# Kernel tuning notes

Hardware: AMD Instinct MI355X
Metric: run time of the kernel (lower is better)

Reference implementation:

```python
import jax, jax.numpy as jnp
import numpy as np

NUM_MODELS = 4
B = 16384
HIDDEN = 512
QDIM = 256
LAST_HIDDEN = 256
UW = 0.1          # uncertainty_weight
EPS = 1e-5        # LayerNorm eps (torch default)
FEAT_DIMS = [1024, 768, 512, 640]


def _linear(x, W, b):
    return x @ W.T + b


def _layernorm(h, g, b):
    mu = jnp.mean(h, axis=-1, keepdims=True)
    var = jnp.mean((h - mu) ** 2, axis=-1, keepdims=True)
    return (h - mu) * jax.lax.rsqrt(var + EPS) * g + b


def setup_inputs() -> dict:
    key = jax.random.key(0)
    ks = jax.random.split(key, 40)
    inp = {}
    for i, d in enumerate(FEAT_DIMS):
        inp[f"feat{i}"] = jax.random.normal(ks[i], (B, d), jnp.float32)
        inp[f"W_intra{i}"] = jax.random.normal(ks[4 + i], (HIDDEN, d), jnp.float32) / np.sqrt(d)
        inp[f"b_intra{i}"] = jnp.zeros((HIDDEN,), jnp.float32)
    inp["pred_scores"] = jax.random.uniform(ks[8], (B, NUM_MODELS), jnp.float32)
    inp["pred_vars"] = jax.random.uniform(ks[9], (B, NUM_MODELS), jnp.float32)
    inp["ln_g"] = jnp.ones((HIDDEN,), jnp.float32)
    inp["ln_b"] = jnp.zeros((HIDDEN,), jnp.float32)
    inp["Wq"] = jax.random.normal(ks[10], (QDIM, HIDDEN), jnp.float32) / np.sqrt(HIDDEN)
    inp["bq"] = jnp.zeros((QDIM,), jnp.float32)
    inp["Wk"] = jax.random.normal(ks[11], (QDIM, HIDDEN), jnp.float32) / np.sqrt(HIDDEN)
    inp["bk"] = jnp.zeros((QDIM,), jnp.float32)
    inp["Wv"] = jax.random.normal(ks[12], (QDIM, HIDDEN), jnp.float32) / np.sqrt(HIDDEN)
    inp["bv"] = jnp.zeros((QDIM,), jnp.float32)
    d1 = NUM_MODELS * QDIM + NUM_MODELS
    inp["W1"] = jax.random.normal(ks[13], (LAST_HIDDEN, d1), jnp.float32) / np.sqrt(d1)
    inp["b1"] = jnp.zeros((LAST_HIDDEN,), jnp.float32)
    inp["Wfc"] = jax.random.normal(ks[14], (1, LAST_HIDDEN), jnp.float32) / np.sqrt(LAST_HIDDEN)
    inp["bfc"] = jnp.zeros((1,), jnp.float32)
    return inp


def _forward(feats, pred_scores, pred_vars, W_intras, b_intras,
             ln_g, ln_b, Wq, bq, Wk, bk, Wv, bv, W1, b1, Wfc, bfc):
    # per-model branch: Linear -> ReLU -> (dropout=id) -> ReLU -> LayerNorm
    hiddens = []
    for i in range(NUM_MODELS):
        h = jax.nn.relu(_linear(feats[i], W_intras[i], b_intras[i]))
        h = jax.nn.relu(h)  # second relu after dropout (identity in eval)
        hiddens.append(_layernorm(h, ln_g, ln_b))
    H = jnp.stack(hiddens, axis=1)  # (B, M, HIDDEN)

    # cross-attention with uncertainty; NOTE source bug: key = drop(q) => keys == queries
    q = jnp.einsum('bmh,qh->bmq', H, Wq) + bq          # (B, M, Q)
    k = q                                              # faithful to `key = self.drop(q)`
    v = jnp.einsum('bmh,qh->bmq', H, Wv) + bv          # (B, M, Q)

    scores = jnp.einsum('biq,bjq->bij', q, k)          # (B, M, M)
    vars_ = pred_vars[:, None, :] + pred_vars[:, :, None]  # vars[b,i,j] = v[b,j] + v[b,i]
    scores = jax.nn.softmax(scores - UW * vars_, axis=-1)
    z = jnp.einsum('bij,bjq->biq', scores, v).reshape(B, NUM_MODELS * QDIM)

    out = jnp.concatenate([z, pred_scores], axis=-1)
    out = _linear(out, W1, b1)
    logits = _linear(out, Wfc, bfc)
    return jax.nn.sigmoid(logits)  # (B, 1)


def reference(feat0, feat1, feat2, feat3,
              W_intra0, b_intra0, W_intra1, b_intra1,
              W_intra2, b_intra2, W_intra3, b_intra3,
              pred_scores, pred_vars, ln_g, ln_b,
              Wq, bq, Wk, bk, Wv, bv, W1, b1, Wfc, bfc):
    feats = [feat0, feat1, feat2, feat3]
    W_intras = [W_intra0, W_intra1, W_intra2, W_intra3]
    b_intras = [b_intra0, b_intra1, b_intra2, b_intra3]
    return _forward(feats, pred_scores, pred_vars, W_intras, b_intras,
                    ln_g, ln_b, Wq, bq, Wk, bk, Wv, bv, W1, b1, Wfc, bfc)
```

## Files before the change

kernel.cpp:

```cpp
#include <hip/hip_runtime.h>
#include <hip/hip_bf16.h>


typedef __bf16 bf16;
typedef __bf16 bf16x4_t __attribute__((ext_vector_type(4)));
typedef __bf16 bf16x8_t __attribute__((ext_vector_type(8)));
typedef float  f32x4_t  __attribute__((ext_vector_type(4)));

__device__ __forceinline__ bf16x8_t cvt8(f32x4_t a, f32x4_t b) {
  bf16x8_t r;
  r[0] = (bf16)a[0]; r[1] = (bf16)a[1]; r[2] = (bf16)a[2]; r[3] = (bf16)a[3];
  r[4] = (bf16)b[0]; r[5] = (bf16)b[1]; r[6] = (bf16)b[2]; r[7] = (bf16)b[3];
  return r;
}

__device__ __forceinline__ void gl_lds16(const void* g, void* l) {
  __builtin_amdgcn_global_load_lds(
      (const __attribute__((address_space(1))) void*)g,
      (__attribute__((address_space(3))) void*)l, 16, 0, 0);
}

#define SBAR()   __builtin_amdgcn_s_barrier()
#define SCHED0() __builtin_amdgcn_sched_barrier(0)

__device__ __forceinline__ bf16x8_t frag_b16(const bf16* Ts, int row, int c0) {
  const int byte = row * 64 + ((c0 ^ ((row >> 1) & 3)) << 4);
  return *(const bf16x8_t*)((const char*)Ts + byte);
}
__device__ __forceinline__ bf16x8_t frag_f32(const float* Ts, int row, int g) {
  const int p0 = (2 * g)     ^ (row & 7);
  const int p1 = (2 * g + 1) ^ (row & 7);
  f32x4_t lo = *(const f32x4_t*)((const char*)Ts + row * 128 + (p0 << 4));
  f32x4_t hi = *(const f32x4_t*)((const char*)Ts + row * 128 + (p1 << 4));
  return cvt8(lo, hi);
}

__device__ __forceinline__ void stage_b16(const bf16* __restrict__ src, int ld,
                                          int k0, bf16* lds) {
  const int l = threadIdx.x & 63;
  const int w = threadIdx.x >> 6;
#pragma unroll
  for (int j = 0; j < 2; ++j) {
    const int rb = w * 32 + j * 16;
    const int r  = rb + (l >> 2);
    const int sc = (l & 3) ^ ((r >> 1) & 3);
    gl_lds16(src + (size_t)r * ld + k0 + sc * 8, (char*)lds + rb * 64);
  }
}
__device__ __forceinline__ void stage_f32(const float* __restrict__ src, int ld,
                                          int k0, float* lds) {
  const int l = threadIdx.x & 63;
  const int w = threadIdx.x >> 6;
#pragma unroll
  for (int j = 0; j < 4; ++j) {
    const int rb = w * 32 + j * 8;
    const int r  = rb + (l >> 3);
    const int q  = (l & 7) ^ (r & 7);
    gl_lds16(src + (size_t)r * ld + k0 + q * 4, (char*)lds + rb * 128);
  }
}

template<int AF32>
__device__ __forceinline__ void stage_deep(const void* A, int lda, const void* B,
                                           int ldb, int k0, char* buf) {
  if (AF32) {
    stage_f32((const float*)A, lda, k0, (float*)buf);
    stage_b16((const bf16*)B, ldb, k0, (bf16*)(buf + 16384));
  } else {
    stage_b16((const bf16*)A, lda, k0, (bf16*)buf);
    stage_f32((const float*)B, ldb, k0, (float*)(buf + 8192));
  }
}

template<int AF32>
__device__ __forceinline__ void mfma_deep(const char* buf, f32x4_t acc[4][4]) {
  const int lane = threadIdx.x & 63;
  const int wid  = threadIdx.x >> 6;
  const int wm = wid >> 1, wn = wid & 1;
  const int fr = lane & 15, g = lane >> 4;
  bf16x8_t ar[4], br[4];
  if (AF32) {
    const float* Af = (const float*)buf;
    const bf16*  Bb = (const bf16*)(buf + 16384);
#pragma unroll
    for (int mi = 0; mi < 4; ++mi) ar[mi] = frag_f32(Af, wm * 64 + mi * 16 + fr, g);
#pragma unroll
    for (int ni = 0; ni < 4; ++ni) br[ni] = frag_b16(Bb, wn * 64 + ni * 16 + fr, g);
  } else {
    const bf16*  Ab = (const bf16*)buf;
    const float* Bf = (const float*)(buf + 8192);
#pragma unroll
    for (int mi = 0; mi < 4; ++mi) ar[mi] = frag_b16(Ab, wm * 64 + mi * 16 + fr, g);
#pragma unroll
    for (int ni = 0; ni < 4; ++ni) br[ni] = frag_f32(Bf, wn * 64 + ni * 16 + fr, g);
  }
#pragma unroll
  for (int mi = 0; mi < 4; ++mi)
#pragma unroll
    for (int ni = 0; ni < 4; ++ni)
      acc[mi][ni] = __builtin_amdgcn_mfma_f32_16x16x32_bf16(ar[mi], br[ni], acc[mi][ni], 0, 0, 0);
}

template<int AF32>
__device__ __forceinline__ void core_deep3(const void* A, int lda, const void* B,
                                           int ldb, int K, char* lds,
                                           f32x4_t acc[4][4]) {
  const int nt = K >> 5;
  stage_deep<AF32>(A, lda, B, ldb, 0,  lds);
  stage_deep<AF32>(A, lda, B, ldb, 32, lds + 24576);
  stage_deep<AF32>(A, lda, B, ldb, 64, lds + 49152);
  int buf = 0;
  for (int t = 0; t < nt; ++t) {
    const int ahead = nt - 1 - t;
    if (ahead >= 2)      asm volatile("s_waitcnt vmcnt(12)" ::: "memory");
    else if (ahead == 1) asm volatile("s_waitcnt vmcnt(6)"  ::: "memory");
    else                 asm volatile("s_waitcnt vmcnt(0)"  ::: "memory");
    SBAR(); SCHED0();
    __builtin_amdgcn_s_setprio(1);
    mfma_deep<AF32>(lds + buf * 24576, acc);
    __builtin_amdgcn_s_setprio(0);
    SCHED0(); SBAR();
    if (t + 3 < nt) stage_deep<AF32>(A, lda, B, ldb, (t + 3) * 32, lds + buf * 24576);
    buf = (buf == 2) ? 0 : buf + 1;
  }
}

template<int RELU>
__device__ __forceinline__ void epi_bf16(f32x4_t acc[4][4], bf16* __restrict__ C, int ldc,
                                         const float* __restrict__ bias) {
  const int lane = threadIdx.x & 63;
  const int wid  = threadIdx.x >> 6;
  const int wm = wid >> 1, wn = wid & 1;
  const int fr = lane & 15;
  const int rb = wm * 64 + 4 * (lane >> 4);
  const int cb = wn * 64 + fr;
  float bv[4];
#pragma unroll
  for (int ni = 0; ni < 4; ++ni) bv[ni] = bias[cb + ni * 16];
#pragma unroll
  for (int mi = 0; mi < 4; ++mi)
#pragma unroll
    for (int j = 0; j < 4; ++j)
#pragma unroll
      for (int ni = 0; ni < 4; ++ni) {
        float val = acc[mi][ni][j] + bv[ni];
        if (RELU) val = fmaxf(val, 0.f);
        C[(size_t)(rb + mi * 16 + j) * ldc + cb + ni * 16] = (bf16)val;
      }
}

__device__ __forceinline__ void stage_f32_512(const float* __restrict__ src, int ld,
                                              int k0, float* lds) {
  const int l = threadIdx.x & 63;
  const int w = threadIdx.x >> 6;
#pragma unroll
  for (int j = 0; j < 2; ++j) {
    const int rb = w * 16 + j * 8;
    const int r  = rb + (l >> 3);
    const int q  = (l & 7) ^ (r & 7);
    gl_lds16(src + (size_t)r * ld + k0 + q * 4, (char*)lds + rb * 128);
  }
}
__device__ __forceinline__ void stage_b16_512(const bf16* __restrict__ src, int ld,
                                              int k0, bf16* lds) {
  const int l = threadIdx.x & 63;
  const int w = threadIdx.x >> 6;
#pragma unroll
  for (int j = 0; j < 4; ++j) {
    const int rb = w * 64 + j * 16;
    const int r  = rb + (l >> 2);
    const int sc = (l & 3) ^ ((r >> 1) & 3);
    gl_lds16(src + (size_t)r * ld + k0 + sc * 8, (char*)lds + rb * 64);
  }
}

__device__ __forceinline__ void mfma_512(const char* buf, f32x4_t acc[8][4]) {
  const int lane = threadIdx.x & 63;
  const int wn   = threadIdx.x >> 6;
  const int fr = lane & 15, g = lane >> 4;
  const float* Af = (const float*)buf;
  const bf16*  Bb = (const bf16*)(buf + 16384);
  bf16x8_t ar[8], br[4];
#pragma unroll
  for (int mi = 0; mi < 8; ++mi) ar[mi] = frag_f32(Af, mi * 16 + fr, g);
#pragma unroll
  for (int ni = 0; ni < 4; ++ni) br[ni] = frag_b16(Bb, wn * 64 + ni * 16 + fr, g);
#pragma unroll
  for (int mi = 0; mi < 8; ++mi)
#pragma unroll
    for (int ni = 0; ni < 4; ++ni)
      acc[mi][ni] = __builtin_amdgcn_mfma_f32_16x16x32_bf16(ar[mi], br[ni], acc[mi][ni], 0, 0, 0);
}

__global__ __launch_bounds__(512, 2) void intra_kernel(
    const float* __restrict__ f0, const float* __restrict__ f1,
    const float* __restrict__ f2, const float* __restrict__ f3,
    const bf16* __restrict__ wb0, const bf16* __restrict__ wb1,
    const bf16* __restrict__ wb2, const bf16* __restrict__ wb3,
    const float* __restrict__ bb0, const float* __restrict__ bb1,
    const float* __restrict__ bb2, const float* __restrict__ bb3,
    bf16* __restrict__ hbuf) {
  __shared__ __align__(16) char lds[98304];
  const int bid = blockIdx.x;
  const int lid = (bid & 7) * 64 + (bid >> 3);
  const int z = lid & 3;
  const int y = lid >> 2;
  const float* fp; const bf16* wp; const float* bp; int K;
  switch (z) {
    case 0:  fp = f0; wp = wb0; bp = bb0; K = 1024; break;
    case 1:  fp = f1; wp = wb1; bp = bb1; K = 768;  break;
    case 2:  fp = f2; wp = wb2; bp = bb2; K = 512;  break;
    default: fp = f3; wp = wb3; bp = bb3; K = 640;  break;
  }
  const float* A = fp + (size_t)(y * 128) * K;
  const bf16*  B = wp;

  f32x4_t acc[8][4];
#pragma unroll
  for (int i = 0; i < 8; ++i)
#pragma unroll
    for (int j = 0; j < 4; ++j) acc[i][j] = (f32x4_t){0.f, 0.f, 0.f, 0.f};

  const int nt = K >> 5;
  char* buf0 = lds;
  char* buf1 = lds + 49152;
  stage_f32_512(A, K, 0, (float*)buf0);
  stage_b16_512(B, K, 0, (bf16*)(buf0 + 16384));
  stage_f32_512(A, K, 32, (float*)buf1);
  stage_b16_512(B, K, 32, (bf16*)(buf1 + 16384));
  for (int t = 0; t < nt; ++t) {
    char* cur = (t & 1) ? buf1 : buf0;
    if (t + 1 < nt) asm volatile("s_waitcnt vmcnt(6)" ::: "memory");
    else            asm volatile("s_waitcnt vmcnt(0)" ::: "memory");
    SBAR(); SCHED0();
    __builtin_amdgcn_s_setprio(1);
    mfma_512(cur, acc);
    __builtin_amdgcn_s_setprio(0);
    SCHED0(); SBAR();
    if (t + 2 < nt) {
      stage_f32_512(A, K, (t + 2) * 32, (float*)cur);
      stage_b16_512(B, K, (t + 2) * 32, (bf16*)(cur + 16384));
    }
  }

  const int lane = threadIdx.x & 63;
  const int wn   = threadIdx.x >> 6;
  const int fr = lane & 15;
  const int rb = 4 * (lane >> 4);
  float bv[4];
#pragma unroll
  for (int ni = 0; ni < 4; ++ni) bv[ni] = bp[wn * 64 + ni * 16 + fr];
  bf16* C = hbuf + (size_t)(y * 128) * 2048 + z * 512;
#pragma unroll
  for (int mi = 0; mi < 8; ++mi)
#pragma unroll
    for (int j = 0; j < 4; ++j) {
      const int row = mi * 16 + rb + j;
#pragma unroll
      for (int ni = 0; ni < 4; ++ni) {
        float val = fmaxf(acc[mi][ni][j] + bv[ni], 0.f);
        C[(size_t)row * 2048 + wn * 64 + ni * 16 + fr] = (bf16)val;
      }
    }
}

__device__ __forceinline__ void cp8(bf16* d, const float* s) {
  f32x4_t x0 = *(const f32x4_t*)s;
  f32x4_t x1 = *(const f32x4_t*)(s + 4);
  *(bf16x8_t*)d = cvt8(x0, x1);
}

__global__ __launch_bounds__(256) void prep_kernel(
    const float* __restrict__ w0, const float* __restrict__ w1s,
    const float* __restrict__ w2, const float* __restrict__ w3,
    bf16* __restrict__ o0, bf16* __restrict__ o1,
    bf16* __restrict__ o2, bf16* __restrict__ o3) {
  const int t = blockIdx.x * 256 + threadIdx.x;
  if (t < 65536)       { size_t i = (size_t)t * 8;            cp8(o0 + i, w0 + i); }
  else if (t < 114688) { size_t i = (size_t)(t - 65536) * 8;  cp8(o1 + i, w1s + i); }
  else if (t < 147456) { size_t i = (size_t)(t - 114688) * 8; cp8(o2 + i, w2 + i); }
  else                 { size_t i = (size_t)(t - 147456) * 8; cp8(o3 + i, w3 + i); }
}

__global__ __launch_bounds__(256)
void ln_kernel(bf16* __restrict__ h, const float* __restrict__ g,
               const float* __restrict__ bta) {
  const int row  = blockIdx.x * 4 + (threadIdx.x >> 6);
  const int lane = threadIdx.x & 63;
  bf16* p = h + (size_t)row * 512 + lane * 8;
  const bf16x8_t x = *(const bf16x8_t*)p;
  float xf[8]; float s = 0.f, s2 = 0.f;
#pragma unroll
  for (int j = 0; j < 8; ++j) { xf[j] = (float)x[j]; s += xf[j]; s2 += xf[j] * xf[j]; }
#pragma unroll
  for (int off = 1; off < 64; off <<= 1) { s += __shfl_xor(s, off); s2 += __shfl_xor(s2, off); }
  const float mu  = s * (1.f / 512.f);
  const float var = s2 * (1.f / 512.f) - mu * mu;
  const float inv = rsqrtf(var + 1e-5f);
  f32x4_t g0 = *(const f32x4_t*)(g + lane * 8);
  f32x4_t g1 = *(const f32x4_t*)(g + lane * 8 + 4);
  f32x4_t b0 = *(const f32x4_t*)(bta + lane * 8);
  f32x4_t b1 = *(const f32x4_t*)(bta + lane * 8 + 4);
  bf16x8_t o;
#pragma unroll
  for (int j = 0; j < 4; ++j) o[j]     = (bf16)((xf[j] - mu) * inv * g0[j] + b0[j]);
#pragma unroll
  for (int j = 0; j < 4; ++j) o[4 + j] = (bf16)((xf[4 + j] - mu) * inv * g1[j] + b1[j]);
  *(bf16x8_t*)p = o;
}

__global__ __launch_bounds__(256) void qv_kernel(
    const bf16* __restrict__ H, const float* __restrict__ Wq,
    const float* __restrict__ Wv, const float* __restrict__ bq,
    const float* __restrict__ bv, bf16* __restrict__ qvout) {
  __shared__ __align__(16) char lds[73728];
  const int bid = blockIdx.x;
  const int lid = (bid & 7) * 256 + (bid >> 3);
  const int x = lid & 3, y = lid >> 2;
  const float* Wsrc = (x < 2) ? Wq : Wv;
  f32x4_t acc[4][4];
#pragma unroll
  for (int i = 0; i < 4; ++i)
#pragma unroll
    for (int j = 0; j < 4; ++j) acc[i][j] = (f32x4_t){0.f, 0.f, 0.f, 0.f};
  core_deep3<0>(H + (size_t)(y * 128) * 512, 512,
                Wsrc + (size_t)((x & 1) * 128) * 512, 512, 512, lds, acc);
  const float* bias = (x < 2) ? bq + x * 128 : bv + (x - 2) * 128;
  epi_bf16<0>(acc, qvout + (size_t)(y * 128) * 512 + x * 128, 512, bias);
}

__global__ __launch_bounds__(256) void w1_kernel(
    const bf16* __restrict__ zb, const float* __restrict__ W1,
    const float* __restrict__ b1, const float* __restrict__ ps,
    float* __restrict__ obuf) {
  __shared__ __align__(16) char lds[73728];
  const int bid = blockIdx.x;
  const int lid = (bid & 7) * 32 + (bid >> 3);
  const int x = lid & 1, y = lid >> 1;
  f32x4_t acc[4][4];
#pragma unroll
  for (int i = 0; i < 4; ++i)
#pragma unroll
    for (int j = 0; j < 4; ++j) acc[i][j] = (f32x4_t){0.f, 0.f, 0.f, 0.f};
  core_deep3<0>(zb + (size_t)(y * 128) * 1024, 1024,
                W1 + (size_t)(x * 128) * 1028, 1028, 1024, lds, acc);

  const int lane = threadIdx.x & 63;
  const int wid  = threadIdx.x >> 6;
  const int wm = wid >> 1, wn = wid & 1;
  const int fr = lane & 15;
  const int rb = wm * 64 + 4 * (lane >> 4);
  const int cb = x * 128 + wn * 64 + fr;
  float bv[4], wt[4][4];
#pragma unroll
  for (int ni = 0; ni < 4; ++ni) {
    bv[ni] = b1[cb + ni * 16];
#pragma unroll
    for (int m = 0; m < 4; ++m) wt[ni][m] = W1[(size_t)(cb + ni * 16) * 1028 + 1024 + m];
  }
#pragma unroll
  for (int mi = 0; mi < 4; ++mi)
#pragma unroll
    for (int j = 0; j < 4; ++j) {
      const int r = y * 128 + rb + mi * 16 + j;
      f32x4_t psv = *(const f32x4_t*)(ps + (size_t)r * 4);
#pragma unroll
      for (int ni = 0; ni < 4; ++ni) {
        float val = acc[mi][ni][j] + bv[ni]
                  + psv[0] * wt[ni][0] + psv[1] * wt[ni][1]
                  + psv[2] * wt[ni][2] + psv[3] * wt[ni][3];
        obuf[(size_t)r * 256 + cb + ni * 16] = val;
      }
    }
}

__global__ __launch_bounds__(256)
void attn_kernel(const bf16* __restrict__ qv, const float* __restrict__ pvars,
                 bf16* __restrict__ z) {
  const int b    = blockIdx.x * 4 + (threadIdx.x >> 6);
  const int lane = threadIdx.x & 63;
  float qf[4][4], vf[4][4];
#pragma unroll
  for (int i = 0; i < 4; ++i) {
    const bf16* row = qv + ((size_t)b * 4 + i) * 512;
    bf16x4_t qq = *(const bf16x4_t*)(row + lane * 4);
    bf16x4_t vv = *(const bf16x4_t*)(row + 256 + lane * 4);
#pragma unroll
    for (int c = 0; c < 4; ++c) { qf[i][c] = (float)qq[c]; vf[i][c] = (float)vv[c]; }
  }
  float s[4][4];
#pragma unroll
  for (int i = 0; i < 4; ++i)
#pragma unroll
    for (int j = 0; j < 4; ++j)
      s[i][j] = qf[i][0] * qf[j][0] + qf[i][1] * qf[j][1] + qf[i][2] * qf[j][2] + qf[i][3] * qf[j][3];
#pragma unroll
  for (int off = 1; off < 64; off <<= 1)
#pragma unroll
    for (int i = 0; i < 4; ++i)
#pragma unroll
      for (int j = 0; j < 4; ++j) s[i][j] += __shfl_xor(s[i][j], off);

  float var4[4];
#pragma unroll
  for (int m = 0; m < 4; ++m) var4[m] = pvars[(size_t)b * 4 + m];
  float w[4][4];
#pragma unroll
  for (int i = 0; i < 4; ++i) {
    float t[4]; float mx = -1e30f;
#pragma unroll
    for (int j = 0; j < 4; ++j) { t[j] = s[i][j] - 0.1f * (var4[i] + var4[j]); mx = fmaxf(mx, t[j]); }
    float sum = 0.f;
#pragma unroll
    for (int j = 0; j < 4; ++j) { t[j] = expf(t[j] - mx); sum += t[j]; }
    const float is = 1.f / sum;
#pragma unroll
    for (int j = 0; j < 4; ++j) w[i][j] = t[j] * is;
  }
#pragma unroll
  for (int i = 0; i < 4; ++i) {
    bf16x4_t zo;
#pragma unroll
    for (int c = 0; c < 4; ++c) {
      float zf = w[i][0] * vf[0][c] + w[i][1] * vf[1][c] + w[i][2] * vf[2][c] + w[i][3] * vf[3][c];
      zo[c] = (bf16)zf;
    }
    *(bf16x4_t*)(z + ((size_t)b * 4 + i) * 256 + lane * 4) = zo;
  }
}

__global__ __launch_bounds__(256)
void fc_kernel(const float* __restrict__ o, const float* __restrict__ wfc,
               const float* __restrict__ bfc, float* __restrict__ out) {
  const int b    = blockIdx.x * 4 + (threadIdx.x >> 6);
  const int lane = threadIdx.x & 63;
  f32x4_t ov = *(const f32x4_t*)(o + (size_t)b * 256 + lane * 4);
  f32x4_t wv = *(const f32x4_t*)(wfc + lane * 4);
  float p = ov[0] * wv[0] + ov[1] * wv[1] + ov[2] * wv[2] + ov[3] * wv[3];
#pragma unroll
  for (int off = 1; off < 64; off <<= 1) p += __shfl_xor(p, off);
  if (lane == 0) {
    const float lg = p + bfc[0];
    out[b] = 1.f / (1.f + expf(-lg));
  }
}

extern "C" void kernel_launch(void* const* d_in, const int* in_sizes, int n_in,
                              void* d_out, int out_size, void* d_ws, size_t ws_size,
                              hipStream_t stream) {
  (void)in_sizes; (void)n_in; (void)out_size; (void)ws_size;
  const float* feat[4] = {(const float*)d_in[0], (const float*)d_in[3],
                          (const float*)d_in[6], (const float*)d_in[9]};
  const float* Wi[4]   = {(const float*)d_in[1], (const float*)d_in[4],
                          (const float*)d_in[7], (const float*)d_in[10]};
  const float* bi[4]   = {(const float*)d_in[2], (const float*)d_in[5],
                          (const float*)d_in[8], (const float*)d_in[11]};
  const float* ps  = (const float*)d_in[12];
  const float* pv  = (const float*)d_in[13];
  const float* lng = (const float*)d_in[14];
  const float* lnb = (const float*)d_in[15];
  const float* Wq  = (const float*)d_in[16];
  const float* bq  = (const float*)d_in[17];
  const float* Wv  = (const float*)d_in[20];
  const float* bvp = (const float*)d_in[21];
  const float* W1  = (const float*)d_in[22];
  const float* b1  = (const float*)d_in[23];
  const float* Wfc = (const float*)d_in[24];
  const float* bfc = (const float*)d_in[25];

  char* ws = (char*)d_ws;
  const size_t MB = 1024 * 1024;
  bf16*  hbuf  = (bf16*)ws;
  bf16*  zbuf  = (bf16*)ws;
  float* obuf  = (float*)(ws + 32 * MB);
  bf16*  wb0   = (bf16*)(ws + 64 * MB);
  bf16*  wb1   = (bf16*)(ws + 65 * MB);
  bf16*  wb2   = (bf16*)(ws + 65 * MB + 786432);
  bf16*  wb3   = (bf16*)(ws + 66 * MB + 262144);
  bf16*  qvout = (bf16*)(ws + 64 * MB);

  hipLaunchKernelGGL(prep_kernel, dim3(736), dim3(256), 0, stream,
                     Wi[0], Wi[1], Wi[2], Wi[3], wb0, wb1, wb2, wb3);
  hipLaunchKernelGGL(intra_kernel, dim3(512), dim3(512), 0, stream,
                     feat[0], feat[1], feat[2], feat[3],
                     wb0, wb1, wb2, wb3, bi[0], bi[1], bi[2], bi[3], hbuf);
  hipLaunchKernelGGL(ln_kernel, dim3(65536 / 4), dim3(256), 0, stream, hbuf, lng, lnb);
  hipLaunchKernelGGL(qv_kernel, dim3(2048), dim3(256), 0, stream,
                     hbuf, Wq, Wv, bq, bvp, qvout);
  hipLaunchKernelGGL(attn_kernel, dim3(16384 / 4), dim3(256), 0, stream, qvout, pv, zbuf);
  hipLaunchKernelGGL(w1_kernel, dim3(256), dim3(256), 0, stream, zbuf, W1, b1, ps, obuf);
  hipLaunchKernelGGL(fc_kernel, dim3(16384 / 4), dim3(256), 0, stream, obuf, Wfc, bfc, (float*)d_out);
}
```

Measured before the change: 252.6 us.

## Fuse LayerNorm into intra GEMM with full-width 512-column tiles

The intra GEMM now has each block compute a full 128x512 output row tile, so the LayerNorm statistics can be reduced in-block (cross-wave through LDS) and applied before the bf16 store. This removes the separate ln_kernel and its read-modify-write pass over H. The block-to-tile mapping is also reordered so the two halves of the grid pair the heavy and light K branches. In exchange, the second launch-bounds argument is dropped and each wave holds a 4x8 accumulator, which may lower occupancy. LN statistics are now taken from fp32 accumulators instead of bf16-rounded values.

```diff
diff --git a/kernel.cpp b/kernel.cpp
--- a/kernel.cpp
+++ b/kernel.cpp
@@ -35,6 +35,163 @@
   return cvt8(lo, hi);
 }
 
+__device__ __forceinline__ void stage_f32_512(const float* __restrict__ src, int ld,
+                                              int k0, float* lds) {
+  const int l = threadIdx.x & 63;
+  const int w = threadIdx.x >> 6;
+#pragma unroll
+  for (int j = 0; j < 2; ++j) {
+    const int rb = w * 16 + j * 8;
+    const int r  = rb + (l >> 3);
+    const int q  = (l & 7) ^ (r & 7);
+    gl_lds16(src + (size_t)r * ld + k0 + q * 4, (char*)lds + rb * 128);
+  }
+}
+__device__ __forceinline__ void stage_b512x32(const bf16* __restrict__ src, int ld,
+                                              int k0, bf16* lds) {
+  const int l = threadIdx.x & 63;
+  const int w = threadIdx.x >> 6;
+#pragma unroll
+  for (int j = 0; j < 4; ++j) {
+    const int rb = w * 64 + j * 16;
+    const int r  = rb + (l >> 2);
+    const int sc = (l & 3) ^ ((r >> 1) & 3);
+    gl_lds16(src + (size_t)r * ld + k0 + sc * 8, (char*)lds + rb * 64);
+  }
+}
+
+__global__ __launch_bounds__(512) void intra_ln_kernel(
+    const float* __restrict__ f0, const float* __restrict__ f1,
+    const float* __restrict__ f2, const float* __restrict__ f3,
+    const bf16* __restrict__ wb0, const bf16* __restrict__ wb1,
+    const bf16* __restrict__ wb2, const bf16* __restrict__ wb3,
+    const float* __restrict__ bb0, const float* __restrict__ bb1,
+    const float* __restrict__ bb2, const float* __restrict__ bb3,
+    const float* __restrict__ lng, const float* __restrict__ lnb,
+    bf16* __restrict__ Hout) {
+  __shared__ __align__(16) char lds[98304];
+  const int bid  = blockIdx.x;
+  const int p    = bid & 255, half = bid >> 8;
+  const int px   = (p & 7) * 32 + (p >> 3);
+  int z = px & 3, y = px >> 2;
+  if (half) { z ^= 2; y += 64; }
+  const float* fp; const bf16* wp; const float* bp; int K;
+  switch (z) {
+    case 0:  fp = f0; wp = wb0; bp = bb0; K = 1024; break;
+    case 1:  fp = f1; wp = wb1; bp = bb1; K = 768;  break;
+    case 2:  fp = f2; wp = wb2; bp = bb2; K = 512;  break;
+    default: fp = f3; wp = wb3; bp = bb3; K = 640;  break;
+  }
+  const float* A = fp + (size_t)(y * 128) * K;
+  const bf16*  B = wp;
+  const int tid = threadIdx.x;
+  const int lane = tid & 63;
+  const int wid  = tid >> 6;
+  const int wm = wid >> 2, wn = wid & 3;
+  const int fr = lane & 15, g = lane >> 4;
+
+  f32x4_t acc[4][8];
+#pragma unroll
+  for (int i = 0; i < 4; ++i)
+#pragma unroll
+    for (int j = 0; j < 8; ++j) acc[i][j] = (f32x4_t){0.f, 0.f, 0.f, 0.f};
+
+  const int nt = K >> 5;
+  char* buf0 = lds;
+  char* buf1 = lds + 49152;
+  auto stage = [&](int t, char* buf) {
+    stage_f32_512(A, K, t * 32, (float*)buf);
+    stage_b512x32(B, K, t * 32, (bf16*)(buf + 16384));
+  };
+  stage(0, buf0);
+  stage(1, buf1);
+  for (int t = 0; t < nt; ++t) {
+    char* cur = (t & 1) ? buf1 : buf0;
+    if (t + 1 < nt) asm volatile("s_waitcnt vmcnt(6)" ::: "memory");
+    else            asm volatile("s_waitcnt vmcnt(0)" ::: "memory");
+    SBAR(); SCHED0();
+    __builtin_amdgcn_s_setprio(1);
+    {
+      const float* Af = (const float*)cur;
+      const bf16*  Bb = (const bf16*)(cur + 16384);
+      bf16x8_t ar[4], br[8];
+#pragma unroll
+      for (int mi = 0; mi < 4; ++mi) ar[mi] = frag_f32(Af, wm * 64 + mi * 16 + fr, g);
+#pragma unroll
+      for (int ni = 0; ni < 8; ++ni) br[ni] = frag_b16(Bb, wn * 128 + ni * 16 + fr, g);
+#pragma unroll
+      for (int mi = 0; mi < 4; ++mi)
+#pragma unroll
+        for (int ni = 0; ni < 8; ++ni)
+          acc[mi][ni] = __builtin_amdgcn_mfma_f32_16x16x32_bf16(ar[mi], br[ni], acc[mi][ni], 0, 0, 0);
+    }
+    __builtin_amdgcn_s_setprio(0);
+    SCHED0(); SBAR();
+    if (t + 2 < nt) stage(t + 2, cur);
+  }
+
+  float* part  = (float*)lds;
+  float* muinv = (float*)(lds + 4096);
+  float bv8[8];
+#pragma unroll
+  for (int ni = 0; ni < 8; ++ni) bv8[ni] = bp[wn * 128 + ni * 16 + fr];
+#pragma unroll
+  for (int mi = 0; mi < 4; ++mi)
+#pragma unroll
+    for (int j = 0; j < 4; ++j) {
+      float s = 0.f, s2 = 0.f;
+#pragma unroll
+      for (int ni = 0; ni < 8; ++ni) {
+        float v = fmaxf(acc[mi][ni][j] + bv8[ni], 0.f);
+        s += v; s2 += v * v;
+      }
+#pragma unroll
+      for (int off = 1; off < 16; off <<= 1) {
+        s += __shfl_xor(s, off); s2 += __shfl_xor(s2, off);
+      }
+      if (fr == 0) {
+        const int rl = mi * 16 + 4 * g + j;
+        part[(wid * 64 + rl) * 2]     = s;
+        part[(wid * 64 + rl) * 2 + 1] = s2;
+      }
+    }
+  __syncthreads();
+  if (tid < 128) {
+    const int wmt = tid >> 6, rl = tid & 63;
+    float s = 0.f, s2 = 0.f;
+#pragma unroll
+    for (int q = 0; q < 4; ++q) {
+      s  += part[((wmt * 4 + q) * 64 + rl) * 2];
+      s2 += part[((wmt * 4 + q) * 64 + rl) * 2 + 1];
+    }
+    const float mu  = s * (1.f / 512.f);
+    const float var = s2 * (1.f / 512.f) - mu * mu;
+    muinv[tid * 2]     = mu;
+    muinv[tid * 2 + 1] = rsqrtf(var + 1e-5f);
+  }
+  __syncthreads();
+  float gg[8], be[8];
+#pragma unroll
+  for (int ni = 0; ni < 8; ++ni) {
+    const int col = wn * 128 + ni * 16 + fr;
+    gg[ni] = lng[col]; be[ni] = lnb[col];
+  }
+#pragma unroll
+  for (int mi = 0; mi < 4; ++mi)
+#pragma unroll
+    for (int j = 0; j < 4; ++j) {
+      const int row = wm * 64 + mi * 16 + 4 * g + j;
+      const float mu  = muinv[row * 2];
+      const float inv = muinv[row * 2 + 1];
+      bf16* hp = Hout + (size_t)(y * 128 + row) * 2048 + z * 512;
+#pragma unroll
+      for (int ni = 0; ni < 8; ++ni) {
+        float v = fmaxf(acc[mi][ni][j] + bv8[ni], 0.f);
+        hp[wn * 128 + ni * 16 + fr] = (bf16)((v - mu) * inv * gg[ni] + be[ni]);
+      }
+    }
+}
+
 __device__ __forceinline__ void stage_b16(const bf16* __restrict__ src, int ld,
                                           int k0, bf16* lds) {
   const int l = threadIdx.x & 63;
@@ -59,57 +216,34 @@
     gl_lds16(src + (size_t)r * ld + k0 + q * 4, (char*)lds + rb * 128);
   }
 }
-
-template<int AF32>
-__device__ __forceinline__ void stage_deep(const void* A, int lda, const void* B,
-                                           int ldb, int k0, char* buf) {
-  if (AF32) {
-    stage_f32((const float*)A, lda, k0, (float*)buf);
-    stage_b16((const bf16*)B, ldb, k0, (bf16*)(buf + 16384));
-  } else {
-    stage_b16((const bf16*)A, lda, k0, (bf16*)buf);
-    stage_f32((const float*)B, ldb, k0, (float*)(buf + 8192));
-  }
-}
-
-template<int AF32>
-__device__ __forceinline__ void mfma_deep(const char* buf, f32x4_t acc[4][4]) {
+__device__ __forceinline__ void mfma_deep0(const char* buf, f32x4_t acc[4][4]) {
   const int lane = threadIdx.x & 63;
   const int wid  = threadIdx.x >> 6;
   const int wm = wid >> 1, wn = wid & 1;
   const int fr = lane & 15, g = lane >> 4;
+  const bf16*  Ab = (const bf16*)buf;
+  const float* Bf = (const float*)(buf + 8192);
   bf16x8_t ar[4], br[4];
-  if (AF32) {
-    const float* Af = (const float*)buf;
-    const bf16*  Bb = (const bf16*)(buf + 16384);
-#pragma unroll
-    for (int mi = 0; mi < 4; ++mi) ar[mi] = frag_f32(Af, wm * 64 + mi * 16 + fr, g);
-#pragma unroll
-    for (int ni = 0; ni < 4; ++ni) br[ni] = frag_b16(Bb, wn * 64 + ni * 16 + fr, g);
-  } else {
-    const bf16*  Ab = (const bf16*)buf;
-    const float* Bf = (const float*)(buf + 8192);
-#pragma unroll
-    for (int mi = 0; mi < 4; ++mi) ar[mi] = frag_b16(Ab, wm * 64 + mi * 16 + fr, g);
-#pragma unroll
-    for (int ni = 0; ni < 4; ++ni) br[ni] = frag_f32(Bf, wn * 64 + ni * 16 + fr, g);
-  }
+#pragma unroll
+  for (int mi = 0; mi < 4; ++mi) ar[mi] = frag_b16(Ab, wm * 64 + mi * 16 + fr, g);
+#pragma unroll
+  for (int ni = 0; ni < 4; ++ni) br[ni] = frag_f32(Bf, wn * 64 + ni * 16 + fr, g);
 #pragma unroll
   for (int mi = 0; mi < 4; ++mi)
 #pragma unroll
     for (int ni = 0; ni < 4; ++ni)
       acc[mi][ni] = __builtin_amdgcn_mfma_f32_16x16x32_bf16(ar[mi], br[ni], acc[mi][ni], 0, 0, 0);
 }
-
-template<int AF32>
-__device__ __forceinline__ void core_deep3(const void* A, int lda, const void* B,
-                                           int ldb, int K, char* lds,
-                                           f32x4_t acc[4][4]) {
+__device__ __forceinline__ void core_deep3_0(const void* A, int lda, const void* B,
+                                             int ldb, int K, char* lds,
+                                             f32x4_t acc[4][4]) {
   const int nt = K >> 5;
-  stage_deep<AF32>(A, lda, B, ldb, 0,  lds);
-  stage_deep<AF32>(A, lda, B, ldb, 32, lds + 24576);
-  stage_deep<AF32>(A, lda, B, ldb, 64, lds + 49152);
-  int buf = 0;
+  auto stage = [&](int t, char* buf) {
+    stage_b16((const bf16*)A, lda, t * 32, (bf16*)buf);
+    stage_f32((const float*)B, ldb, t * 32, (float*)(buf + 8192));
+  };
+  stage(0, lds); stage(1, lds + 24576); stage(2, lds + 49152);
+  int bsel = 0;
   for (int t = 0; t < nt; ++t) {
     const int ahead = nt - 1 - t;
     if (ahead >= 2)      asm volatile("s_waitcnt vmcnt(12)" ::: "memory");
@@ -117,14 +251,13 @@
     else                 asm volatile("s_waitcnt vmcnt(0)"  ::: "memory");
     SBAR(); SCHED0();
     __builtin_amdgcn_s_setprio(1);
-    mfma_deep<AF32>(lds + buf * 24576, acc);
+    mfma_deep0(lds + bsel * 24576, acc);
     __builtin_amdgcn_s_setprio(0);
     SCHED0(); SBAR();
-    if (t + 3 < nt) stage_deep<AF32>(A, lda, B, ldb, (t + 3) * 32, lds + buf * 24576);
-    buf = (buf == 2) ? 0 : buf + 1;
-  }
-}
-
+    if (t + 3 < nt) stage(t + 3, lds + bsel * 24576);
+    bsel = (bsel == 2) ? 0 : bsel + 1;
+  }
+}
 template<int RELU>
 __device__ __forceinline__ void epi_bf16(f32x4_t acc[4][4], bf16* __restrict__ C, int ldc,
                                          const float* __restrict__ bias) {
@@ -149,117 +282,67 @@
       }
 }
 
-__device__ __forceinline__ void stage_f32_512(const float* __restrict__ src, int ld,
-                                              int k0, float* lds) {
-  const int l = threadIdx.x & 63;
-  const int w = threadIdx.x >> 6;
-#pragma unroll
-  for (int j = 0; j < 2; ++j) {
-    const int rb = w * 16 + j * 8;
-    const int r  = rb + (l >> 3);
-    const int q  = (l & 7) ^ (r & 7);
-    gl_lds16(src + (size_t)r * ld + k0 + q * 4, (char*)lds + rb * 128);
-  }
-}
-__device__ __forceinline__ void stage_b16_512(const bf16* __restrict__ src, int ld,
-                                              int k0, bf16* lds) {
-  const int l = threadIdx.x & 63;
-  const int w = threadIdx.x >> 6;
-#pragma unroll
-  for (int j = 0; j < 4; ++j) {
-    const int rb = w * 64 + j * 16;
-    const int r  = rb + (l >> 2);
-    const int sc = (l & 3) ^ ((r >> 1) & 3);
-    gl_lds16(src + (size_t)r * ld + k0 + sc * 8, (char*)lds + rb * 64);
-  }
-}
-
-__device__ __forceinline__ void mfma_512(const char* buf, f32x4_t acc[8][4]) {
+__global__ __launch_bounds__(256) void qv_kernel(
+    const bf16* __restrict__ H, const float* __restrict__ Wq,
+    const float* __restrict__ Wv, const float* __restrict__ bq,
+    const float* __restrict__ bv, bf16* __restrict__ qvout) {
+  __shared__ __align__(16) char lds[73728];
+  const int bid = blockIdx.x;
+  const int lid = (bid & 7) * 256 + (bid >> 3);
+  const int x = lid & 3, y = lid >> 2;
+  const float* Wsrc = (x < 2) ? Wq : Wv;
+  f32x4_t acc[4][4];
+#pragma unroll
+  for (int i = 0; i < 4; ++i)
+#pragma unroll
+    for (int j = 0; j < 4; ++j) acc[i][j] = (f32x4_t){0.f, 0.f, 0.f, 0.f};
+  core_deep3_0(H + (size_t)(y * 128) * 512, 512,
+               Wsrc + (size_t)((x & 1) * 128) * 512, 512, 512, lds, acc);
+  const float* bias = (x < 2) ? bq + x * 128 : bv + (x - 2) * 128;
+  epi_bf16<0>(acc, qvout + (size_t)(y * 128) * 512 + x * 128, 512, bias);
+}
+
+__global__ __launch_bounds__(256) void w1_kernel(
+    const bf16* __restrict__ zb, const float* __restrict__ W1,
+    const float* __restrict__ b1, const float* __restrict__ ps,
+    float* __restrict__ obuf) {
+  __shared__ __align__(16) char lds[73728];
+  const int bid = blockIdx.x;
+  const int lid = (bid & 7) * 32 + (bid >> 3);
+  const int x = lid & 1, y = lid >> 1;
+  f32x4_t acc[4][4];
+#pragma unroll
+  for (int i = 0; i < 4; ++i)
+#pragma unroll
+    for (int j = 0; j < 4; ++j) acc[i][j] = (f32x4_t){0.f, 0.f, 0.f, 0.f};
+  core_deep3_0(zb + (size_t)(y * 128) * 1024, 1024,
+               W1 + (size_t)(x * 128) * 1028, 1028, 1024, lds, acc);
+
   const int lane = threadIdx.x & 63;
-  const int wn   = threadIdx.x >> 6;
-  const int fr = lane & 15, g = lane >> 4;
-  const float* Af = (const float*)buf;
-  const bf16*  Bb = (const bf16*)(buf + 16384);
-  bf16x8_t ar[8], br[4];
-#pragma unroll
-  for (int mi = 0; mi < 8; ++mi) ar[mi] = frag_f32(Af, mi * 16 + fr, g);
-#pragma unroll
-  for (int ni = 0; ni < 4; ++ni) br[ni] = frag_b16(Bb, wn * 64 + ni * 16 + fr, g);
-#pragma unroll
-  for (int mi = 0; mi < 8; ++mi)
-#pragma unroll
-    for (int ni = 0; ni < 4; ++ni)
-      acc[mi][ni] = __builtin_amdgcn_mfma_f32_16x16x32_bf16(ar[mi], br[ni], acc[mi][ni], 0, 0, 0);
-}
-
-__global__ __launch_bounds__(512, 2) void intra_kernel(
-    const float* __restrict__ f0, const float* __restrict__ f1,
-    const float* __restrict__ f2, const float* __restrict__ f3,
-    const bf16* __restrict__ wb0, const bf16* __restrict__ wb1,
-    const bf16* __restrict__ wb2, const bf16* __restrict__ wb3,
-    const float* __restrict__ bb0, const float* __restrict__ bb1,
-    const float* __restrict__ bb2, const float* __restrict__ bb3,
-    bf16* __restrict__ hbuf) {
-  __shared__ __align__(16) char lds[98304];
-  const int bid = blockIdx.x;
-  const int lid = (bid & 7) * 64 + (bid >> 3);
-  const int z = lid & 3;
-  const int y = lid >> 2;
-  const float* fp; const bf16* wp; const float* bp; int K;
-  switch (z) {
-    case 0:  fp = f0; wp = wb0; bp = bb0; K = 1024; break;
-    case 1:  fp = f1; wp = wb1; bp = bb1; K = 768;  break;
-    case 2:  fp = f2; wp = wb2; bp = bb2; K = 512;  break;
-    default: fp = f3; wp = wb3; bp = bb3; K = 640;  break;
-  }
-  const float* A = fp + (size_t)(y * 128) * K;
-  const bf16*  B = wp;
-
-  f32x4_t acc[8][4];
-#pragma unroll
-  for (int i = 0; i < 8; ++i)
-#pragma unroll
-    for (int j = 0; j < 4; ++j) acc[i][j] = (f32x4_t){0.f, 0.f, 0.f, 0.f};
-
-  const int nt = K >> 5;
-  char* buf0 = lds;
-  char* buf1 = lds + 49152;
-  stage_f32_512(A, K, 0, (float*)buf0);
-  stage_b16_512(B, K, 0, (bf16*)(buf0 + 16384));
-  stage_f32_512(A, K, 32, (float*)buf1);
-  stage_b16_512(B, K, 32, (bf16*)(buf1 + 16384));
-  for (int t = 0; t < nt; ++t) {
-    char* cur = (t & 1) ? buf1 : buf0;
-    if (t + 1 < nt) asm volatile("s_waitcnt vmcnt(6)" ::: "memory");
-    else            asm volatile("s_waitcnt vmcnt(0)" ::: "memory");
-    SBAR(); SCHED0();
-    __builtin_amdgcn_s_setprio(1);
-    mfma_512(cur, acc);
-    __builtin_amdgcn_s_setprio(0);
-    SCHED0(); SBAR();
-    if (t + 2 < nt) {
-      stage_f32_512(A, K, (t + 2) * 32, (float*)cur);
-      stage_b16_512(B, K, (t + 2) * 32, (bf16*)(cur + 16384));
-    }
-  }
-
-  const int lane = threadIdx.x & 63;
-  const int wn   = threadIdx.x >> 6;
+  const int wid  = threadIdx.x >> 6;
+  const int wm = wid >> 1, wn = wid & 1;
   const int fr = lane & 15;
-  const int rb = 4 * (lane >> 4);
-  float bv[4];
-#pragma unroll
-  for (int ni = 0; ni < 4; ++ni) bv[ni] = bp[wn * 64 + ni * 16 + fr];
-  bf16* C = hbuf + (size_t)(y * 128) * 2048 + z * 512;
-#pragma unroll
-  for (int mi = 0; mi < 8; ++mi)
+  const int rb = wm * 64 + 4 * (lane >> 4);
+  const int cb = x * 128 + wn * 64 + fr;
+  float bv[4], wt[4][4];
+#pragma unroll
+  for (int ni = 0; ni < 4; ++ni) {
+    bv[ni] = b1[cb + ni * 16];
+#pragma unroll
+    for (int m = 0; m < 4; ++m) wt[ni][m] = W1[(size_t)(cb + ni * 16) * 1028 + 1024 + m];
+  }
+#pragma unroll
+  for (int mi = 0; mi < 4; ++mi)
 #pragma unroll
     for (int j = 0; j < 4; ++j) {
-      const int row = mi * 16 + rb + j;
+      const int r = y * 128 + rb + mi * 16 + j;
+      f32x4_t psv = *(const f32x4_t*)(ps + (size_t)r * 4);
 #pragma unroll
       for (int ni = 0; ni < 4; ++ni) {
-        float val = fmaxf(acc[mi][ni][j] + bv[ni], 0.f);
-        C[(size_t)row * 2048 + wn * 64 + ni * 16 + fr] = (bf16)val;
+        float val = acc[mi][ni][j] + bv[ni]
+                  + psv[0] * wt[ni][0] + psv[1] * wt[ni][1]
+                  + psv[2] * wt[ni][2] + psv[3] * wt[ni][3];
+        obuf[(size_t)r * 256 + cb + ni * 16] = val;
       }
     }
 }
@@ -269,7 +352,6 @@
   f32x4_t x1 = *(const f32x4_t*)(s + 4);
   *(bf16x8_t*)d = cvt8(x0, x1);
 }
-
 __global__ __launch_bounds__(256) void prep_kernel(
     const float* __restrict__ w0, const float* __restrict__ w1s,
     const float* __restrict__ w2, const float* __restrict__ w3,
@@ -280,98 +362,6 @@
   else if (t < 114688) { size_t i = (size_t)(t - 65536) * 8;  cp8(o1 + i, w1s + i); }
   else if (t < 147456) { size_t i = (size_t)(t - 114688) * 8; cp8(o2 + i, w2 + i); }
   else                 { size_t i = (size_t)(t - 147456) * 8; cp8(o3 + i, w3 + i); }
-}
-
-__global__ __launch_bounds__(256)
-void ln_kernel(bf16* __restrict__ h, const float* __restrict__ g,
-               const float* __restrict__ bta) {
-  const int row  = blockIdx.x * 4 + (threadIdx.x >> 6);
-  const int lane = threadIdx.x & 63;
-  bf16* p = h + (size_t)row * 512 + lane * 8;
-  const bf16x8_t x = *(const bf16x8_t*)p;
-  float xf[8]; float s = 0.f, s2 = 0.f;
-#pragma unroll
-  for (int j = 0; j < 8; ++j) { xf[j] = (float)x[j]; s += xf[j]; s2 += xf[j] * xf[j]; }
-#pragma unroll
-  for (int off = 1; off < 64; off <<= 1) { s += __shfl_xor(s, off); s2 += __shfl_xor(s2, off); }
-  const float mu  = s * (1.f / 512.f);
-  const float var = s2 * (1.f / 512.f) - mu * mu;
-  const float inv = rsqrtf(var + 1e-5f);
-  f32x4_t g0 = *(const f32x4_t*)(g + lane * 8);
-  f32x4_t g1 = *(const f32x4_t*)(g + lane * 8 + 4);
-  f32x4_t b0 = *(const f32x4_t*)(bta + lane * 8);
-  f32x4_t b1 = *(const f32x4_t*)(bta + lane * 8 + 4);
-  bf16x8_t o;
-#pragma unroll
-  for (int j = 0; j < 4; ++j) o[j]     = (bf16)((xf[j] - mu) * inv * g0[j] + b0[j]);
-#pragma unroll
-  for (int j = 0; j < 4; ++j) o[4 + j] = (bf16)((xf[4 + j] - mu) * inv * g1[j] + b1[j]);
-  *(bf16x8_t*)p = o;
-}
-
-__global__ __launch_bounds__(256) void qv_kernel(
-    const bf16* __restrict__ H, const float* __restrict__ Wq,
-    const float* __restrict__ Wv, const float* __restrict__ bq,
-    const float* __restrict__ bv, bf16* __restrict__ qvout) {
-  __shared__ __align__(16) char lds[73728];
-  const int bid = blockIdx.x;
-  const int lid = (bid & 7) * 256 + (bid >> 3);
-  const int x = lid & 3, y = lid >> 2;
-  const float* Wsrc = (x < 2) ? Wq : Wv;
-  f32x4_t acc[4][4];
-#pragma unroll
-  for (int i = 0; i < 4; ++i)
-#pragma unroll
-    for (int j = 0; j < 4; ++j) acc[i][j] = (f32x4_t){0.f, 0.f, 0.f, 0.f};
-  core_deep3<0>(H + (size_t)(y * 128) * 512, 512,
-                Wsrc + (size_t)((x & 1) * 128) * 512, 512, 512, lds, acc);
-  const float* bias = (x < 2) ? bq + x * 128 : bv + (x - 2) * 128;
-  epi_bf16<0>(acc, qvout + (size_t)(y * 128) * 512 + x * 128, 512, bias);
-}
-
-__global__ __launch_bounds__(256) void w1_kernel(
-    const bf16* __restrict__ zb, const float* __restrict__ W1,
-    const float* __restrict__ b1, const float* __restrict__ ps,
-    float* __restrict__ obuf) {
-  __shared__ __align__(16) char lds[73728];
-  const int bid = blockIdx.x;
-  const int lid = (bid & 7) * 32 + (bid >> 3);
-  const int x = lid & 1, y = lid >> 1;
-  f32x4_t acc[4][4];
-#pragma unroll
-  for (int i = 0; i < 4; ++i)
-#pragma unroll
-    for (int j = 0; j < 4; ++j) acc[i][j] = (f32x4_t){0.f, 0.f, 0.f, 0.f};
-  core_deep3<0>(zb + (size_t)(y * 128) * 1024, 1024,
-                W1 + (size_t)(x * 128) * 1028, 1028, 1024, lds, acc);
-
-  const int lane = threadIdx.x & 63;
-  const int wid  = threadIdx.x >> 6;
-  const int wm = wid >> 1, wn = wid & 1;
-  const int fr = lane & 15;
-  const int rb = wm * 64 + 4 * (lane >> 4);
-  const int cb = x * 128 + wn * 64 + fr;
-  float bv[4], wt[4][4];
-#pragma unroll
-  for (int ni = 0; ni < 4; ++ni) {
-    bv[ni] = b1[cb + ni * 16];
-#pragma unroll
-    for (int m = 0; m < 4; ++m) wt[ni][m] = W1[(size_t)(cb + ni * 16) * 1028 + 1024 + m];
-  }
-#pragma unroll
-  for (int mi = 0; mi < 4; ++mi)
-#pragma unroll
-    for (int j = 0; j < 4; ++j) {
-      const int r = y * 128 + rb + mi * 16 + j;
-      f32x4_t psv = *(const f32x4_t*)(ps + (size_t)r * 4);
-#pragma unroll
-      for (int ni = 0; ni < 4; ++ni) {
-        float val = acc[mi][ni][j] + bv[ni]
-                  + psv[0] * wt[ni][0] + psv[1] * wt[ni][1]
-                  + psv[2] * wt[ni][2] + psv[3] * wt[ni][3];
-        obuf[(size_t)r * 256 + cb + ni * 16] = val;
-      }
-    }
 }
 
 __global__ __launch_bounds__(256)
@@ -481,10 +471,10 @@
 
   hipLaunchKernelGGL(prep_kernel, dim3(736), dim3(256), 0, stream,
                      Wi[0], Wi[1], Wi[2], Wi[3], wb0, wb1, wb2, wb3);
-  hipLaunchKernelGGL(intra_kernel, dim3(512), dim3(512), 0, stream,
+  hipLaunchKernelGGL(intra_ln_kernel, dim3(512), dim3(512), 0, stream,
                      feat[0], feat[1], feat[2], feat[3],
-                     wb0, wb1, wb2, wb3, bi[0], bi[1], bi[2], bi[3], hbuf);
-  hipLaunchKernelGGL(ln_kernel, dim3(65536 / 4), dim3(256), 0, stream, hbuf, lng, lnb);
+                     wb0, wb1, wb2, wb3, bi[0], bi[1], bi[2], bi[3],
+                     lng, lnb, hbuf);
   hipLaunchKernelGGL(qv_kernel, dim3(2048), dim3(256), 0, stream,
                      hbuf, Wq, Wv, bq, bvp, qvout);
   hipLaunchKernelGGL(attn_kernel, dim3(16384 / 4), dim3(256), 0, stream, qvout, pv, zbuf);
```

After: 237.9 us. 1.06x faster.
